# Performance work log

Hardware: AMD Instinct MI355X
Metric: run time of the kernel (lower is better)

Reference implementation:

```python
import jax, jax.numpy as jnp
import numpy as np

CLIP_LIMIT = 40.0
GRID = (8, 8)
NUM_BINS = 256


def setup_inputs() -> dict:
    key = jax.random.key(0)
    # CLAHE expects image values in [0, 1]
    x = jax.random.uniform(key, (8, 3, 1024, 1024), dtype=jnp.float32)
    return {"x": x}


def _interp_coords(n_tiles, tile_size, length):
    """Per-pixel tile-pair indices and blend weight along one axis.

    Follows kornia's half-tile interpolation grid: pixels in the first/last
    half-tile use only the nearest tile LUT; interior pixels blend the two
    nearest tile LUTs with weights linear over a full tile span (denom 2*half-1).
    """
    half = tile_size // 2
    pos = jnp.arange(length)
    j = pos // half          # interpolation-tile row/col index (0 .. 2*n_tiles-1)
    p = pos % half           # offset within the half tile
    r0 = jnp.clip((j - 1) // 2, 0, n_tiles - 1)
    r1 = jnp.clip(r0 + 1, 0, n_tiles - 1)
    denom = float(2 * half - 1)
    w = jnp.where(j % 2 == 1, (2 * half - 1) - p, (half - 1) - p).astype(jnp.float32) / denom
    w = jnp.where(j == 0, 1.0, w)  # first half-tile: nearest LUT only
    return r0, r1, w


def _clahe(x):
    B, C, H, W = x.shape
    GH, GW = GRID
    th = -(-H // GH); th += th % 2   # even tile height (kornia even_tile_size=True)
    tw = -(-W // GW); tw += tw % 2
    Hp, Wp = th * GH, tw * GW
    xp = jnp.pad(x, ((0, 0), (0, 0), (0, Hp - H), (0, Wp - W)), mode='reflect') if (Hp > H or Wp > W) else x

    # tiles: B x C x GH x GW x th x tw
    tiles = xp.reshape(B, C, GH, th, GW, tw).transpose(0, 1, 2, 4, 3, 5)
    pixels = th * tw
    T = B * C * GH * GW

    # per-tile 256-bin histogram (histc over [0,1] -> floor(x*256), last bin closed)
    bins = jnp.clip((tiles * NUM_BINS).astype(jnp.int32), 0, NUM_BINS - 1).reshape(T, pixels)
    hist = jnp.zeros((T, NUM_BINS), jnp.float32).at[jnp.arange(T)[:, None], bins].add(1.0)

    # clip + uniform redistribution of the excess (kornia scheme)
    if CLIP_LIMIT > 0:
        max_val = max(CLIP_LIMIT * pixels // NUM_BINS, 1.0)
        hist = jnp.minimum(hist, max_val)
        clipped = pixels - hist.sum(axis=1)                 # excess per tile
        residual = jnp.mod(clipped, NUM_BINS)
        hist = hist + ((clipped - residual) / NUM_BINS)[:, None]
        hist = hist + (jnp.arange(NUM_BINS)[None, :] < residual[:, None]).astype(jnp.float32)

    # LUT from CDF, floored to emulate integer conversion
    lut_scale = (NUM_BINS - 1) / pixels
    lut = jnp.floor(jnp.clip(jnp.cumsum(hist, axis=1) * lut_scale, 0, NUM_BINS - 1))
    lut = lut.reshape(B, C, GH, GW, NUM_BINS)

    # per-pixel LUT lookup index (kornia uses (x*255).long())
    idx = jnp.clip((xp * 255.0).astype(jnp.int32), 0, 255)

    r0, r1, wy = _interp_coords(GH, th, Hp)
    c0, c1, wx = _interp_coords(GW, tw, Wp)

    b_i = jnp.arange(B)[:, None, None, None]
    ch_i = jnp.arange(C)[None, :, None, None]

    def g(ry, cx):
        # gather lut[b, c, ry(y), cx(x), idx[b,c,y,x]] -> (B, C, Hp, Wp)
        return lut[b_i, ch_i, ry[None, None, :, None], cx[None, None, None, :], idx]

    wy2 = wy[:, None]
    wx2 = wx[None, :]
    out = (wy2 * wx2 * g(r0, c0)
           + wy2 * (1.0 - wx2) * g(r0, c1)
           + (1.0 - wy2) * wx2 * g(r1, c0)
           + (1.0 - wy2) * (1.0 - wx2) * g(r1, c1))
    return out[..., :H, :W] / 255.0


def reference(x):
    return _clahe(x)
```

## Files before the change

### kernel.cpp

```cpp
#include <hip/hip_runtime.h>

#define NBINS 256
#define TILE  128
#define CLIPV 2560u

__global__ __launch_bounds__(256) void clahe_hist_lut(
        const float* __restrict__ x, float* __restrict__ lut) {
    const int t   = blockIdx.x;
    const int tid = threadIdx.x;

    __shared__ unsigned int hs[NBINS * 8];
    __shared__ int          scan[2][NBINS];
    __shared__ unsigned int wsum[4];

    #pragma unroll
    for (int k = 0; k < 8; ++k) hs[k * NBINS + tid] = 0u;
    __syncthreads();

    const int tx = t & 7;
    const int ty = (t >> 3) & 7;
    const int bc = t >> 6;
    const float* base = x + ((size_t)bc * 1024 + (size_t)ty * TILE) * 1024
                          + (size_t)tx * TILE;

    const int sub    = tid & 7;
    const int lane32 = tid & 31;
    const int rgrp   = tid >> 5;
    #pragma unroll 4
    for (int rr = 0; rr < 16; ++rr) {
        const int row = rr * 8 + rgrp;
        const float4 v = *(const float4*)(base + (size_t)row * 1024 + lane32 * 4);
        int b0 = min(max((int)(v.x * 256.0f), 0), 255);
        int b1 = min(max((int)(v.y * 256.0f), 0), 255);
        int b2 = min(max((int)(v.z * 256.0f), 0), 255);
        int b3 = min(max((int)(v.w * 256.0f), 0), 255);
        atomicAdd(&hs[b0 * 8 + sub], 1u);
        atomicAdd(&hs[b1 * 8 + sub], 1u);
        atomicAdd(&hs[b2 * 8 + sub], 1u);
        atomicAdd(&hs[b3 * 8 + sub], 1u);
    }
    __syncthreads();

    const uint4* hp = (const uint4*)(&hs[tid * 8]);
    const uint4 ha = hp[0], hb = hp[1];
    const unsigned int total = ha.x + ha.y + ha.z + ha.w
                             + hb.x + hb.y + hb.z + hb.w;
    const unsigned int hv = min(total, CLIPV);
    unsigned int e = total - hv;
    #pragma unroll
    for (int off = 32; off > 0; off >>= 1) e += __shfl_down(e, off, 64);
    if ((tid & 63) == 0) wsum[tid >> 6] = e;
    __syncthreads();
    const unsigned int E        = wsum[0] + wsum[1] + wsum[2] + wsum[3];
    const unsigned int add      = E >> 8;
    const unsigned int residual = E & 255u;
    const int h2 = (int)(hv + add + ((unsigned)tid < residual ? 1u : 0u));

    scan[0][tid] = h2;
    __syncthreads();
    int src = 0;
    #pragma unroll
    for (int off = 1; off < 256; off <<= 1) {
        int v = scan[src][tid];
        if (tid >= off) v += scan[src][tid - off];
        scan[src ^ 1][tid] = v;
        __syncthreads();
        src ^= 1;
    }
    const int cum = scan[src][tid];
    const float l = fminf((float)cum * (255.0f / 16384.0f), 255.0f);
    lut[(size_t)t * NBINS + tid] = floorf(l);
}

__global__ __launch_bounds__(256) void clahe_apply(
        const float* __restrict__ x, const float* __restrict__ lut,
        float* __restrict__ out) {
    __shared__ float l0[8 * NBINS];
    __shared__ float l1[8 * NBINS];

    const int blk = blockIdx.x;
    const int bc  = blk >> 7;
    const int rg  = blk & 127;
    const int y0  = rg * 8;
    const int tid = threadIdx.x;

    const int j = y0 >> 6;
    int r0 = (j - 1) >> 1;
    r0 = min(max(r0, 0), 7);
    const int r1 = min(r0 + 1, 7);

    {
        const float* lb = lut + (size_t)bc * 64 * NBINS;
        const float4* s0 = (const float4*)(lb + (size_t)r0 * 8 * NBINS);
        const float4* s1 = (const float4*)(lb + (size_t)r1 * 8 * NBINS);
        ((float4*)l0)[tid]       = s0[tid];
        ((float4*)l0)[tid + 256] = s0[tid + 256];
        ((float4*)l1)[tid]       = s1[tid];
        ((float4*)l1)[tid + 256] = s1[tid + 256];
    }
    __syncthreads();

    int c0k[4], c1k[4];
    float wxk[4];
    #pragma unroll
    for (int k = 0; k < 4; ++k) {
        const int xx = tid * 4 + k;
        const int jc = xx >> 6, pc = xx & 63;
        int c0 = (jc - 1) >> 1;
        c0 = min(max(c0, 0), 7);
        c0k[k] = c0;
        c1k[k] = min(c0 + 1, 7);
        wxk[k] = (jc == 0) ? 1.0f
               : (float)((jc & 1) ? (127 - pc) : (63 - pc)) / 127.0f;
    }

    const bool jzero = (j == 0);
    const bool jodd  = (j & 1);
    const size_t rowbase = ((size_t)bc * 1024 + (size_t)y0) * 1024 + tid * 4;

    #pragma unroll
    for (int r = 0; r < 8; ++r) {
        const int p = (y0 + r) & 63;
        const float wy = jzero ? 1.0f
                       : (float)(jodd ? (127 - p) : (63 - p)) / 127.0f;

        const float4 v = *(const float4*)(x + rowbase + (size_t)r * 1024);
        const float vv[4] = {v.x, v.y, v.z, v.w};
        float res[4];
        #pragma unroll
        for (int k = 0; k < 4; ++k) {
            const int idx = min(max((int)(vv[k] * 255.0f), 0), 255);
            const int o0 = c0k[k] * NBINS + idx;
            const int o1 = c1k[k] * NBINS + idx;
            const float g00 = l0[o0];
            const float g01 = l0[o1];
            const float g10 = l1[o0];
            const float g11 = l1[o1];
            const float wx = wxk[k];
            const float o = wy * wx * g00 + wy * (1.0f - wx) * g01
                          + (1.0f - wy) * wx * g10 + (1.0f - wy) * (1.0f - wx) * g11;
            res[k] = o / 255.0f;
        }
        *(float4*)(out + rowbase + (size_t)r * 1024) =
            make_float4(res[0], res[1], res[2], res[3]);
    }
}

extern "C" void kernel_launch(void* const* d_in, const int* in_sizes, int n_in,
                              void* d_out, int out_size, void* d_ws, size_t ws_size,
                              hipStream_t stream) {
    const float* x = (const float*)d_in[0];
    float* out = (float*)d_out;
    float* lut = (float*)d_ws;

    clahe_hist_lut<<<1536, 256, 0, stream>>>(x, lut);
    clahe_apply<<<24 * 128, 256, 0, stream>>>(x, lut, out);
}
```

Measured before the change: 195.9 us.

## Interleave row LUT pairs in shared memory, double rows per block, nontemporal IO

Stores the two row-tile LUTs interleaved in shared memory so each pixel does two 8-byte LDS reads instead of four 4-byte reads. The blend is rewritten as nested FMA lerps with a multiply by the reciprocal instead of a divide. Each apply block now covers 16 rows instead of 8, halving the number of blocks and the LUT staging per row. Input loads and output stores use nontemporal hints to reduce cache pollution. The FMA form may differ slightly in rounding from the reference, and fewer blocks means less parallelism.

```diff
diff --git a/kernel.cpp b/kernel.cpp
--- a/kernel.cpp
+++ b/kernel.cpp
@@ -3,6 +3,9 @@
 #define NBINS 256
 #define TILE  128
 #define CLIPV 2560u
+
+typedef float  fx4 __attribute__((ext_vector_type(4)));
+typedef float  fx2 __attribute__((ext_vector_type(2)));
 
 __global__ __launch_bounds__(256) void clahe_hist_lut(
         const float* __restrict__ x, float* __restrict__ lut) {
@@ -29,7 +32,8 @@
     #pragma unroll 4
     for (int rr = 0; rr < 16; ++rr) {
         const int row = rr * 8 + rgrp;
-        const float4 v = *(const float4*)(base + (size_t)row * 1024 + lane32 * 4);
+        const fx4 v = __builtin_nontemporal_load(
+            (const fx4*)(base + (size_t)row * 1024 + lane32 * 4));
         int b0 = min(max((int)(v.x * 256.0f), 0), 255);
         int b1 = min(max((int)(v.y * 256.0f), 0), 255);
         int b2 = min(max((int)(v.z * 256.0f), 0), 255);
@@ -75,13 +79,12 @@
 __global__ __launch_bounds__(256) void clahe_apply(
         const float* __restrict__ x, const float* __restrict__ lut,
         float* __restrict__ out) {
-    __shared__ float l0[8 * NBINS];
-    __shared__ float l1[8 * NBINS];
+    __shared__ fx4 l01s[1024];
 
     const int blk = blockIdx.x;
-    const int bc  = blk >> 7;
-    const int rg  = blk & 127;
-    const int y0  = rg * 8;
+    const int bc  = blk >> 6;
+    const int rg  = blk & 63;
+    const int y0  = rg * 16;
     const int tid = threadIdx.x;
 
     const int j = y0 >> 6;
@@ -91,16 +94,21 @@
 
     {
         const float* lb = lut + (size_t)bc * 64 * NBINS;
-        const float4* s0 = (const float4*)(lb + (size_t)r0 * 8 * NBINS);
-        const float4* s1 = (const float4*)(lb + (size_t)r1 * 8 * NBINS);
-        ((float4*)l0)[tid]       = s0[tid];
-        ((float4*)l0)[tid + 256] = s0[tid + 256];
-        ((float4*)l1)[tid]       = s1[tid];
-        ((float4*)l1)[tid + 256] = s1[tid + 256];
+        const fx4* s0 = (const fx4*)(lb + (size_t)r0 * 8 * NBINS);
+        const fx4* s1 = (const fx4*)(lb + (size_t)r1 * 8 * NBINS);
+        #pragma unroll
+        for (int e = 0; e < 2; ++e) {
+            const int i4 = e * 256 + tid;
+            const fx4 a = s0[i4];
+            const fx4 b = s1[i4];
+            l01s[i4 * 2]     = (fx4){a.x, b.x, a.y, b.y};
+            l01s[i4 * 2 + 1] = (fx4){a.z, b.z, a.w, b.w};
+        }
     }
     __syncthreads();
+    const fx2* lv = (const fx2*)l01s;
 
-    int c0k[4], c1k[4];
+    int o0k[4], o1k[4];
     float wxk[4];
     #pragma unroll
     for (int k = 0; k < 4; ++k) {
@@ -108,8 +116,8 @@
         const int jc = xx >> 6, pc = xx & 63;
         int c0 = (jc - 1) >> 1;
         c0 = min(max(c0, 0), 7);
-        c0k[k] = c0;
-        c1k[k] = min(c0 + 1, 7);
+        o0k[k] = c0 * NBINS;
+        o1k[k] = min(c0 + 1, 7) * NBINS;
         wxk[k] = (jc == 0) ? 1.0f
                : (float)((jc & 1) ? (127 - pc) : (63 - pc)) / 127.0f;
     }
@@ -118,31 +126,29 @@
     const bool jodd  = (j & 1);
     const size_t rowbase = ((size_t)bc * 1024 + (size_t)y0) * 1024 + tid * 4;
 
-    #pragma unroll
-    for (int r = 0; r < 8; ++r) {
+    #pragma unroll 4
+    for (int r = 0; r < 16; ++r) {
         const int p = (y0 + r) & 63;
         const float wy = jzero ? 1.0f
                        : (float)(jodd ? (127 - p) : (63 - p)) / 127.0f;
 
-        const float4 v = *(const float4*)(x + rowbase + (size_t)r * 1024);
+        const fx4 v = __builtin_nontemporal_load(
+            (const fx4*)(x + rowbase + (size_t)r * 1024));
         const float vv[4] = {v.x, v.y, v.z, v.w};
         float res[4];
         #pragma unroll
         for (int k = 0; k < 4; ++k) {
             const int idx = min(max((int)(vv[k] * 255.0f), 0), 255);
-            const int o0 = c0k[k] * NBINS + idx;
-            const int o1 = c1k[k] * NBINS + idx;
-            const float g00 = l0[o0];
-            const float g01 = l0[o1];
-            const float g10 = l1[o0];
-            const float g11 = l1[o1];
+            const fx2 G0 = lv[o0k[k] + idx];
+            const fx2 G1 = lv[o1k[k] + idx];
             const float wx = wxk[k];
-            const float o = wy * wx * g00 + wy * (1.0f - wx) * g01
-                          + (1.0f - wy) * wx * g10 + (1.0f - wy) * (1.0f - wx) * g11;
-            res[k] = o / 255.0f;
+            const float a = fmaf(wx, G0.x - G1.x, G1.x);
+            const float b = fmaf(wx, G0.y - G1.y, G1.y);
+            res[k] = fmaf(wy, a - b, b) * (1.0f / 255.0f);
         }
-        *(float4*)(out + rowbase + (size_t)r * 1024) =
-            make_float4(res[0], res[1], res[2], res[3]);
+        const fx4 o4 = {res[0], res[1], res[2], res[3]};
+        __builtin_nontemporal_store(
+            o4, (fx4*)(out + rowbase + (size_t)r * 1024));
     }
 }
 
@@ -154,5 +160,5 @@
     float* lut = (float*)d_ws;
 
     clahe_hist_lut<<<1536, 256, 0, stream>>>(x, lut);
-    clahe_apply<<<24 * 128, 256, 0, stream>>>(x, lut, out);
+    clahe_apply<<<24 * 64, 256, 0, stream>>>(x, lut, out);
 }
```

Result: faster. 190.0 us (-3.0%).
